# Optimization experiments

Hardware: AMD Instinct MI355X
Metric: run time of the kernel (lower is better)

Reference implementation:

```python
import jax, jax.numpy as jnp
import numpy as np

N = 100_000      # nodes
E = 1_600_000    # edges (before self-loops)
IN_C = 500
HID = 128
OUT_C = 64
L = 8
ALPHA = 0.1
THETA = 0.5


def setup_inputs() -> dict:
    key = jax.random.key(0)
    ks = jax.random.split(key, 6)
    x = jax.random.normal(ks[0], (N, IN_C), dtype=jnp.float32)
    edge_index = jax.random.randint(ks[1], (2, E), 0, N, dtype=jnp.int32)
    s0 = 1.0 / np.sqrt(IN_C)
    W_in = jax.random.uniform(ks[2], (IN_C, HID), jnp.float32, -s0, s0)
    b_in = jnp.zeros((HID,), jnp.float32)
    sh = 1.0 / np.sqrt(HID)
    W_conv = jax.random.uniform(ks[3], (L, HID, HID), jnp.float32, -sh, sh)
    W_out = jax.random.uniform(ks[4], (HID, OUT_C), jnp.float32, -sh, sh)
    b_out = jnp.zeros((OUT_C,), jnp.float32)
    return {"x": x, "edge_index": edge_index, "W_in": W_in, "b_in": b_in,
            "W_conv": W_conv, "W_out": W_out, "b_out": b_out}


def reference(x, edge_index, W_in, b_in, W_conv, W_out, b_out):
    # dropout is identity in eval mode
    loop = jnp.arange(N, dtype=edge_index.dtype)
    src = jnp.concatenate([edge_index[0], loop])  # add self-loops (gcn_norm)
    dst = jnp.concatenate([edge_index[1], loop])
    deg = jax.ops.segment_sum(jnp.ones_like(src, dtype=x.dtype), dst, num_segments=N)
    dinv = jnp.where(deg > 0, jax.lax.rsqrt(deg), 0.0)
    norm = dinv[src] * dinv[dst]  # symmetric normalization coeffs per edge

    h = jax.nn.relu(x @ W_in + b_in)
    h0 = h  # initial residual
    for l in range(L):
        beta = float(np.log(THETA / (l + 1) + 1.0))
        agg = jax.ops.segment_sum(h[src] * norm[:, None], dst, num_segments=N)  # Ahat @ h
        z = (1.0 - ALPHA) * agg + ALPHA * h0
        h = jax.nn.relu((1.0 - beta) * z + beta * (z @ W_conv[l]))
    return h @ W_out + b_out
```

## Files before the change

### kernel.cpp

```cpp
#include <hip/hip_runtime.h>
#include <hip/hip_fp16.h>
#include <cmath>

#define NN 100000
#define EE 1600000
#define INC 500
#define HIDC 128
#define OUTC 64
#define NLAYER 8
#define NB16 6250
#define NPX 12500
#define GEMM_BLKS 782
#define CNT_BLKS 50000
#define FG_BLKS (GEMM_BLKS + CNT_BLKS)

typedef float f32x4 __attribute__((ext_vector_type(4)));
typedef _Float16 f16x8 __attribute__((ext_vector_type(8)));
typedef _Float16 f16x4 __attribute__((ext_vector_type(4)));
typedef short s16x8 __attribute__((ext_vector_type(8)));

__device__ __forceinline__ int fraddr(int row, int k, int Kp) {
  return (row >> 4) * (Kp * 16) + (k >> 3) * 128 + (row & 15) * 8 + (k & 7);
}


__global__ void __launch_bounds__(256) k_count_x(
    const int* __restrict__ dst, int* __restrict__ deg) {
  int chunk = blockIdx.x >> 3;
  int xcd = blockIdx.x & 7;
  int e = chunk * 256 + threadIdx.x;
  int d = dst[e];
  if (d / NPX == xcd) atomicAdd(&deg[d], 1);
}

__global__ void k_scan_block_sums(const int* __restrict__ deg, int* __restrict__ bsum, int n) {
  __shared__ int sm[256];
  int i = blockIdx.x * 256 + threadIdx.x;
  int v = (i < n) ? deg[i] + 1 : 0;
  sm[threadIdx.x] = v;
  __syncthreads();
  for (int s = 128; s > 0; s >>= 1) {
    if (threadIdx.x < s) sm[threadIdx.x] += sm[threadIdx.x + s];
    __syncthreads();
  }
  if (threadIdx.x == 0) bsum[blockIdx.x] = sm[0];
}

__global__ void k_scan_partials(int* __restrict__ bsum, int nb) {
  __shared__ int sm[512];
  int t = threadIdx.x;
  sm[t] = (t < nb) ? bsum[t] : 0;
  __syncthreads();
  for (int s = 1; s < 512; s <<= 1) {
    int v = (t >= s) ? sm[t - s] : 0;
    __syncthreads();
    sm[t] += v;
    __syncthreads();
  }
  if (t < nb) bsum[t] = (t == 0) ? 0 : sm[t - 1];
}

__global__ void k_scan_final(const int* __restrict__ deg, const int* __restrict__ bsum,
                             int* __restrict__ row_ptr, int n) {
  __shared__ int sm[256];
  int i = blockIdx.x * 256 + threadIdx.x;
  int v = (i < n) ? deg[i] + 1 : 0;
  sm[threadIdx.x] = v;
  __syncthreads();
  for (int s = 1; s < 256; s <<= 1) {
    int u = (threadIdx.x >= s) ? sm[threadIdx.x - s] : 0;
    __syncthreads();
    sm[threadIdx.x] += u;
    __syncthreads();
  }
  if (i < n) row_ptr[i] = bsum[blockIdx.x] + sm[threadIdx.x] - v;
}

__global__ void k_init_rows(const int* __restrict__ deg, const int* __restrict__ row_ptr,
                            int* __restrict__ cursor, int* __restrict__ col,
                            float* __restrict__ dinv, int n) {
  int i = blockIdx.x * blockDim.x + threadIdx.x;
  if (i < n) {
    int rp = row_ptr[i];
    col[rp] = i;
    cursor[i] = rp + 1;
    dinv[i] = rsqrtf((float)(deg[i] + 1));
  }
}


__global__ void k_prep_wfin16(const float* __restrict__ W, __half* __restrict__ f) {
  int i = blockIdx.x * 256 + threadIdx.x;
  if (i >= HIDC * 512) return;
  int n = i / 512, k = i % 512;
  float v = (k < INC) ? W[(size_t)k * HIDC + n] : 0.f;
  f[fraddr(n, k, 512)] = __float2half(v);
}


__global__ void k_prep_wf16(const float* __restrict__ W, __half* __restrict__ f,
                            int K, int N, float idc, float ws) {
  int i = blockIdx.x * 256 + threadIdx.x;
  if (i >= N * K) return;
  int n = i / K, k = i % K;
  float v = ws * W[(size_t)k * N + n] + ((k == n) ? idc : 0.f);
  f[fraddr(n, k, K)] = __float2half(v);
}


__global__ void __launch_bounds__(256) k_fill_gemm(
    const int* __restrict__ src, const int* __restrict__ dst,
    int* __restrict__ cursor, int* __restrict__ col,
    const float* __restrict__ A, const __half* __restrict__ Bf,
    const float* __restrict__ bias,
    __half* __restrict__ C16u, __half* __restrict__ C16s,
    const float* __restrict__ dinv) {
  __shared__ __align__(16) _Float16 Ax[128 * 40];
  int bid = blockIdx.x;
  int tid = threadIdx.x;

  if (bid >= GEMM_BLKS) {
    int chunk = (bid - GEMM_BLKS) >> 3;
    int xcd = bid & 7;
    int e = chunk * 256 + tid;
    int d = dst[e];
    if (d / NPX == xcd) {
      int pos = atomicAdd(&cursor[d], 1);
      col[pos] = src[e];
    }
    return;
  }

  int wid = tid >> 6, lane = tid & 63;
  int wr = wid >> 1, wc = wid & 1;
  int lr = lane & 15, kg = lane >> 4;
  int row0 = bid * 128;

  f32x4 acc[4][4];
#pragma unroll
  for (int m = 0; m < 4; ++m)
#pragma unroll
    for (int n = 0; n < 4; ++n) acc[m][n] = {0.f, 0.f, 0.f, 0.f};

  float4 va[4];
  auto issue_loads = [&](int kt) {
#pragma unroll
    for (int p = 0; p < 4; ++p) {
      int idx = tid + p * 256;
      int r = idx >> 3, kq = idx & 7;
      int gr = row0 + r, gk = kt + kq * 4;
      va[p] = make_float4(0.f, 0.f, 0.f, 0.f);
      if (gr < NN && gk < INC) va[p] = *reinterpret_cast<const float4*>(&A[(size_t)gr * INC + gk]);
    }
  };

  issue_loads(0);
  for (int kt = 0; kt < 512; kt += 32) {
#pragma unroll
    for (int p = 0; p < 4; ++p) {
      int idx = tid + p * 256;
      int r = idx >> 3, kq = idx & 7;
      const float* vp = &va[p].x;
      f16x4 h4;
#pragma unroll
      for (int e = 0; e < 4; ++e) h4[e] = (_Float16)vp[e];
      *reinterpret_cast<f16x4*>(&Ax[r * 40 + kq * 4]) = h4;
    }
    __syncthreads();
    if (kt + 32 < 512) issue_loads(kt + 32);

    f16x8 af[4];
#pragma unroll
    for (int m = 0; m < 4; ++m) {
      int r = wr * 64 + m * 16 + lr;
      af[m] = *reinterpret_cast<const f16x8*>(&Ax[r * 40 + kg * 8]);
    }
#pragma unroll
    for (int n = 0; n < 4; ++n) {
      size_t bb = (size_t)(wc * 4 + n) * 8192 + (size_t)(kt / 8 + kg) * 128 + lr * 8;
      f16x8 b = *reinterpret_cast<const f16x8*>(&Bf[bb]);
#pragma unroll
      for (int m = 0; m < 4; ++m)
        acc[m][n] = __builtin_amdgcn_mfma_f32_16x16x32_f16(af[m], b, acc[m][n], 0, 0, 0);
    }
    __syncthreads();
  }

#pragma unroll
  for (int m = 0; m < 4; ++m) {
#pragma unroll
    for (int n = 0; n < 4; ++n) {
      int gc = wc * 64 + n * 16 + lr;
#pragma unroll
      for (int q = 0; q < 4; ++q) {
        int gr = row0 + wr * 64 + m * 16 + kg * 4 + q;
        if (gr < NN) {
          float v = fmaxf(acc[m][n][q] + bias[gc], 0.f);
          C16u[(size_t)gr * HIDC + gc] = __float2half(v);
          C16s[(size_t)gr * HIDC + gc] = __float2half(v * dinv[gr]);
        }
      }
    }
  }
}


template <int EPI>
__global__ void __launch_bounds__(1024) k_layer(
    const __half* __restrict__ hs, const __half* __restrict__ h0u,
    const __half* __restrict__ Bf,
    const int* __restrict__ row_ptr, const int* __restrict__ deg,
    const int* __restrict__ col, const float* __restrict__ dinv,
    __half* __restrict__ Cs,
    const __half* __restrict__ Bf2, const float* __restrict__ bias2,
    float* __restrict__ outp) {
  __shared__ __half zb[16 * 128];
  int wv = threadIdx.x >> 6, lane = threadIdx.x & 63;
  int g = lane >> 4;
  int fl = lane & 15;
  int row0 = blockIdx.x * 16;
  int node = row0 + wv;

  int start = row_ptr[node];
  int cnt = deg[node] + 1;

  float acc[8];
#pragma unroll
  for (int j = 0; j < 8; ++j) acc[j] = 0.f;

  for (int base = 0; base < cnt; base += 64) {
    int rem = cnt - base;
    if (rem > 64) rem = 64;
    int myc = col[start + base + (lane < rem ? lane : 0)];
    int nch = (rem + 3) >> 2;

    auto get = [&](int ch, s16x8& v, float& m) {
      int e = ch * 4 + g;
      int c = __shfl(myc, e & 63, 64);
      m = (e < rem) ? 1.f : 0.f;
      v = *reinterpret_cast<const s16x8*>(&hs[(size_t)c * HIDC + fl * 8]);
    };

    s16x8 curv; float curm;
    get(0, curv, curm);
    for (int ch = 0; ch < nch; ++ch) {
      s16x8 nv = {}; float nm = 0.f;
      if (ch + 1 < nch) get(ch + 1, nv, nm);
      const __half2* hp = reinterpret_cast<const __half2*>(&curv);
#pragma unroll
      for (int j = 0; j < 4; ++j) {
        float2 f = __half22float2(hp[j]);
        acc[2 * j]     = fmaf(curm, f.x, acc[2 * j]);
        acc[2 * j + 1] = fmaf(curm, f.y, acc[2 * j + 1]);
      }
      curv = nv; curm = nm;
    }
  }

#pragma unroll
  for (int j = 0; j < 8; ++j) {
    acc[j] += __shfl_xor(acc[j], 16, 64);
    acc[j] += __shfl_xor(acc[j], 32, 64);
  }

  if (g == 0) {
    float dr = dinv[node] * 0.9f;
    s16x8 r0 = *reinterpret_cast<const s16x8*>(&h0u[(size_t)node * HIDC + fl * 8]);
    const __half2* r0p = reinterpret_cast<const __half2*>(&r0);
    f16x8 w;
#pragma unroll
    for (int j = 0; j < 4; ++j) {
      float2 f0 = __half22float2(r0p[j]);
      w[2 * j]     = (_Float16)fmaf(dr, acc[2 * j],     0.1f * f0.x);
      w[2 * j + 1] = (_Float16)fmaf(dr, acc[2 * j + 1], 0.1f * f0.y);
    }
    *reinterpret_cast<f16x8*>(&zb[wv * 128 + ((fl * 8) ^ ((wv & 7) << 3))]) = w;
  }
  __syncthreads();

  int lr = lane & 15, kg = lane >> 4;
  f32x4 c = {0.f, 0.f, 0.f, 0.f};
  if (wv < 8) {
    const __half* Bb = Bf + wv * 2048 + kg * 128 + lr * 8;
#pragma unroll
    for (int kt = 0; kt < 4; ++kt) {
      f16x8 a = *reinterpret_cast<const f16x8*>(
          &zb[lr * 128 + ((kt * 32 + kg * 8) ^ ((lr & 7) << 3))]);
      f16x8 b = *reinterpret_cast<const f16x8*>(Bb + kt * 512);
      c = __builtin_amdgcn_mfma_f32_16x16x32_f16(a, b, c, 0, 0, 0);
    }
  }

  if (EPI == 0) {
    if (wv < 8) {
      int gc = wv * 16 + lr;
#pragma unroll
      for (int q = 0; q < 4; ++q) {
        int gr = row0 + kg * 4 + q;
        float v = fmaxf(c[q], 0.f);
        Cs[(size_t)gr * HIDC + gc] = __float2half(v * dinv[gr]);
      }
    }
  } else {
    __syncthreads();
    if (wv < 8) {
      int gc = wv * 16 + lr;
#pragma unroll
      for (int q = 0; q < 4; ++q) {
        int r = kg * 4 + q;
        zb[(gc >> 3) * 128 + r * 8 + (gc & 7)] = __float2half(fmaxf(c[q], 0.f));
      }
    }
    __syncthreads();
    if (wv < 4) {
      f32x4 o = {0.f, 0.f, 0.f, 0.f};
      const __half* Bb2 = Bf2 + wv * 2048 + kg * 128 + lr * 8;
#pragma unroll
      for (int kt = 0; kt < 4; ++kt) {
        f16x8 a = *reinterpret_cast<const f16x8*>(&zb[(kt * 4 + kg) * 128 + lr * 8]);
        f16x8 b = *reinterpret_cast<const f16x8*>(Bb2 + kt * 512);
        o = __builtin_amdgcn_mfma_f32_16x16x32_f16(a, b, o, 0, 0, 0);
      }
      int gc = wv * 16 + lr;
      float bv = bias2[gc];
#pragma unroll
      for (int q = 0; q < 4; ++q) {
        int gr = row0 + kg * 4 + q;
        outp[(size_t)gr * OUTC + gc] = o[q] + bv;
      }
    }
  }
}


extern "C" void kernel_launch(void* const* d_in, const int* in_sizes, int n_in,
                              void* d_out, int out_size, void* d_ws, size_t ws_size,
                              hipStream_t stream) {
  const float* x     = (const float*)d_in[0];
  const int*   ei    = (const int*)d_in[1];
  const float* W_in  = (const float*)d_in[2];
  const float* b_in  = (const float*)d_in[3];
  const float* W_cv  = (const float*)d_in[4];
  const float* W_out = (const float*)d_in[5];
  const float* b_out = (const float*)d_in[6];
  float* out = (float*)d_out;

  char* ws = (char*)d_ws;
  size_t off = 0;
  auto alloc = [&](size_t bytes) {
    char* p = ws + off;
    off = (off + bytes + 255) & ~(size_t)255;
    return p;
  };
  int*    deg     = (int*)alloc((size_t)NN * 4);
  int*    row_ptr = (int*)alloc((size_t)NN * 4);
  int*    cursor  = (int*)alloc((size_t)NN * 4);
  int*    bsum    = (int*)alloc(512 * 4);
  float*  dinv    = (float*)alloc((size_t)NN * 4);
  int*    col     = (int*)alloc((size_t)(EE + NN) * 4);
  __half* h016u   = (__half*)alloc((size_t)NN * HIDC * 2);
  __half* h016s   = (__half*)alloc((size_t)NN * HIDC * 2);
  __half* hsA     = (__half*)alloc((size_t)NN * HIDC * 2);
  __half* hsB     = (__half*)alloc((size_t)NN * HIDC * 2);
  __half* wcv16   = (__half*)alloc((size_t)NLAYER * HIDC * HIDC * 2);
  __half* wout16  = (__half*)alloc((size_t)OUTC * HIDC * 2);
  __half* win16   = (__half*)alloc((size_t)HIDC * 512 * 2);

  const int* srcp = ei;
  const int* dstp = ei + EE;

  hipMemsetAsync(deg, 0, (size_t)NN * 4, stream);

  k_prep_wfin16<<<(HIDC * 512 + 255) / 256, 256, 0, stream>>>(W_in, win16);
  for (int l = 0; l < NLAYER; ++l) {
    float beta = logf(0.5f / (float)(l + 1) + 1.0f);
    k_prep_wf16<<<(HIDC * HIDC + 255) / 256, 256, 0, stream>>>(
        W_cv + (size_t)l * HIDC * HIDC, wcv16 + (size_t)l * HIDC * HIDC,
        HIDC, HIDC, 1.0f - beta, beta);
  }
  k_prep_wf16<<<(OUTC * HIDC + 255) / 256, 256, 0, stream>>>(W_out, wout16, HIDC, OUTC,
                                                             0.f, 1.f);

  k_count_x<<<CNT_BLKS, 256, 0, stream>>>(dstp, deg);

  int nb = (NN + 255) / 256;
  k_scan_block_sums<<<nb, 256, 0, stream>>>(deg, bsum, NN);
  k_scan_partials<<<1, 512, 0, stream>>>(bsum, nb);
  k_scan_final<<<nb, 256, 0, stream>>>(deg, bsum, row_ptr, NN);
  k_init_rows<<<(NN + 255) / 256, 256, 0, stream>>>(deg, row_ptr, cursor, col, dinv, NN);

  k_fill_gemm<<<FG_BLKS, 256, 0, stream>>>(srcp, dstp, cursor, col,
                                           x, win16, b_in, h016u, h016s, dinv);

  const __half* hcur = h016s;
  for (int l = 0; l < NLAYER; ++l) {
    const __half* wl = wcv16 + (size_t)l * HIDC * HIDC;
    if (l < NLAYER - 1) {
      __half* tgt = (l & 1) ? hsB : hsA;
      k_layer<0><<<NB16, 1024, 0, stream>>>(hcur, h016u, wl, row_ptr, deg, col, dinv,
                                            tgt, nullptr, nullptr, nullptr);
      hcur = tgt;
    } else {
      k_layer<1><<<NB16, 1024, 0, stream>>>(hcur, h016u, wl, row_ptr, deg, col, dinv,
                                            nullptr, wout16, b_out, out);
    }
  }
}
```

Before: 923.5 us.

## Sort nodes by degree for balanced layer blocks and split fill/GEMM kernel

Builds a degree histogram and a counting-sort permutation so that each 16-node block in the layer kernel handles nodes of similar degree. This reduces wave imbalance inside 1024-thread blocks, where the slowest node sets the block's time. The fused fill+GEMM kernel is also split into two separate kernels. The trade-offs are extra small kernels, indirect perm lookups, and scattered output rows that break write coalescing. Node locality across blocks is also lost.

```diff
diff --git a/kernel.cpp b/kernel.cpp
--- a/kernel.cpp
+++ b/kernel.cpp
@@ -12,7 +12,6 @@
 #define NPX 12500
 #define GEMM_BLKS 782
 #define CNT_BLKS 50000
-#define FG_BLKS (GEMM_BLKS + CNT_BLKS)
 
 typedef float f32x4 __attribute__((ext_vector_type(4)));
 typedef _Float16 f16x8 __attribute__((ext_vector_type(8)));
@@ -89,6 +88,53 @@
 }
 
 
+__global__ void k_hist(const int* __restrict__ deg, int* __restrict__ hist) {
+  __shared__ int lh[64];
+  if (threadIdx.x < 64) lh[threadIdx.x] = 0;
+  __syncthreads();
+  int i = blockIdx.x * 256 + threadIdx.x;
+  if (i < NN) atomicAdd(&lh[min(deg[i], 63)], 1);
+  __syncthreads();
+  if (threadIdx.x < 64 && lh[threadIdx.x]) atomicAdd(&hist[threadIdx.x], lh[threadIdx.x]);
+}
+
+__global__ void k_scan_hist(const int* __restrict__ hist, int* __restrict__ bincur) {
+  __shared__ int sm[64];
+  int t = threadIdx.x;
+  sm[t] = hist[t];
+  __syncthreads();
+  for (int s = 1; s < 64; s <<= 1) {
+    int v = (t >= s) ? sm[t - s] : 0;
+    __syncthreads();
+    sm[t] += v;
+    __syncthreads();
+  }
+  bincur[t] = (t == 0) ? 0 : sm[t - 1];
+}
+
+__global__ void k_perm(const int* __restrict__ deg, int* __restrict__ bincur,
+                       int* __restrict__ perm) {
+  int i = blockIdx.x * 256 + threadIdx.x;
+  if (i < NN) {
+    int p = atomicAdd(&bincur[min(deg[i], 63)], 1);
+    perm[p] = i;
+  }
+}
+
+__global__ void __launch_bounds__(256) k_fill_x(
+    const int* __restrict__ src, const int* __restrict__ dst,
+    int* __restrict__ cursor, int* __restrict__ col) {
+  int chunk = blockIdx.x >> 3;
+  int xcd = blockIdx.x & 7;
+  int e = chunk * 256 + threadIdx.x;
+  int d = dst[e];
+  if (d / NPX == xcd) {
+    int pos = atomicAdd(&cursor[d], 1);
+    col[pos] = src[e];
+  }
+}
+
+
 __global__ void k_prep_wfin16(const float* __restrict__ W, __half* __restrict__ f) {
   int i = blockIdx.x * 256 + threadIdx.x;
   if (i >= HIDC * 512) return;
@@ -108,33 +154,17 @@
 }
 
 
-__global__ void __launch_bounds__(256) k_fill_gemm(
-    const int* __restrict__ src, const int* __restrict__ dst,
-    int* __restrict__ cursor, int* __restrict__ col,
+__global__ void __launch_bounds__(256) k_gemm_in(
     const float* __restrict__ A, const __half* __restrict__ Bf,
     const float* __restrict__ bias,
     __half* __restrict__ C16u, __half* __restrict__ C16s,
     const float* __restrict__ dinv) {
   __shared__ __align__(16) _Float16 Ax[128 * 40];
-  int bid = blockIdx.x;
   int tid = threadIdx.x;
-
-  if (bid >= GEMM_BLKS) {
-    int chunk = (bid - GEMM_BLKS) >> 3;
-    int xcd = bid & 7;
-    int e = chunk * 256 + tid;
-    int d = dst[e];
-    if (d / NPX == xcd) {
-      int pos = atomicAdd(&cursor[d], 1);
-      col[pos] = src[e];
-    }
-    return;
-  }
-
   int wid = tid >> 6, lane = tid & 63;
   int wr = wid >> 1, wc = wid & 1;
   int lr = lane & 15, kg = lane >> 4;
-  int row0 = bid * 128;
+  int row0 = blockIdx.x * 128;
 
   f32x4 acc[4][4];
 #pragma unroll
@@ -211,6 +241,7 @@
     const __half* __restrict__ Bf,
     const int* __restrict__ row_ptr, const int* __restrict__ deg,
     const int* __restrict__ col, const float* __restrict__ dinv,
+    const int* __restrict__ perm,
     __half* __restrict__ Cs,
     const __half* __restrict__ Bf2, const float* __restrict__ bias2,
     float* __restrict__ outp) {
@@ -219,7 +250,7 @@
   int g = lane >> 4;
   int fl = lane & 15;
   int row0 = blockIdx.x * 16;
-  int node = row0 + wv;
+  int node = perm[row0 + wv];
 
   int start = row_ptr[node];
   int cnt = deg[node] + 1;
@@ -296,9 +327,9 @@
       int gc = wv * 16 + lr;
 #pragma unroll
       for (int q = 0; q < 4; ++q) {
-        int gr = row0 + kg * 4 + q;
+        int pr = perm[row0 + kg * 4 + q];
         float v = fmaxf(c[q], 0.f);
-        Cs[(size_t)gr * HIDC + gc] = __float2half(v * dinv[gr]);
+        Cs[(size_t)pr * HIDC + gc] = __float2half(v * dinv[pr]);
       }
     }
   } else {
@@ -325,8 +356,8 @@
       float bv = bias2[gc];
 #pragma unroll
       for (int q = 0; q < 4; ++q) {
-        int gr = row0 + kg * 4 + q;
-        outp[(size_t)gr * OUTC + gc] = o[q] + bv;
+        int pr = perm[row0 + kg * 4 + q];
+        outp[(size_t)pr * OUTC + gc] = o[q] + bv;
       }
     }
   }
@@ -356,6 +387,9 @@
   int*    row_ptr = (int*)alloc((size_t)NN * 4);
   int*    cursor  = (int*)alloc((size_t)NN * 4);
   int*    bsum    = (int*)alloc(512 * 4);
+  int*    hist    = (int*)alloc(64 * 4);
+  int*    bincur  = (int*)alloc(64 * 4);
+  int*    perm    = (int*)alloc((size_t)NN * 4);
   float*  dinv    = (float*)alloc((size_t)NN * 4);
   int*    col     = (int*)alloc((size_t)(EE + NN) * 4);
   __half* h016u   = (__half*)alloc((size_t)NN * HIDC * 2);
@@ -370,6 +404,7 @@
   const int* dstp = ei + EE;
 
   hipMemsetAsync(deg, 0, (size_t)NN * 4, stream);
+  hipMemsetAsync(hist, 0, 64 * 4, stream);
 
   k_prep_wfin16<<<(HIDC * 512 + 255) / 256, 256, 0, stream>>>(W_in, win16);
   for (int l = 0; l < NLAYER; ++l) {
@@ -389,8 +424,13 @@
   k_scan_final<<<nb, 256, 0, stream>>>(deg, bsum, row_ptr, NN);
   k_init_rows<<<(NN + 255) / 256, 256, 0, stream>>>(deg, row_ptr, cursor, col, dinv, NN);
 
-  k_fill_gemm<<<FG_BLKS, 256, 0, stream>>>(srcp, dstp, cursor, col,
-                                           x, win16, b_in, h016u, h016s, dinv);
+  k_hist<<<nb, 256, 0, stream>>>(deg, hist);
+  k_scan_hist<<<1, 64, 0, stream>>>(hist, bincur);
+  k_perm<<<nb, 256, 0, stream>>>(deg, bincur, perm);
+
+  k_fill_x<<<CNT_BLKS, 256, 0, stream>>>(srcp, dstp, cursor, col);
+
+  k_gemm_in<<<GEMM_BLKS, 256, 0, stream>>>(x, win16, b_in, h016u, h016s, dinv);
 
   const __half* hcur = h016s;
   for (int l = 0; l < NLAYER; ++l) {
@@ -398,11 +438,11 @@
     if (l < NLAYER - 1) {
       __half* tgt = (l & 1) ? hsB : hsA;
       k_layer<0><<<NB16, 1024, 0, stream>>>(hcur, h016u, wl, row_ptr, deg, col, dinv,
-                                            tgt, nullptr, nullptr, nullptr);
+                                            perm, tgt, nullptr, nullptr, nullptr);
       hcur = tgt;
     } else {
       k_layer<1><<<NB16, 1024, 0, stream>>>(hcur, h016u, wl, row_ptr, deg, col, dinv,
-                                            nullptr, wout16, b_out, out);
-    }
-  }
-}
+                                            perm, nullptr, wout16, b_out, out);
+    }
+  }
+}
```

Result: slower. 1.193 ms (+29.2%).

## Split fused fill/GEMM kernel and use LDS-free per-wave input GEMM

Applied to the files above, without the earlier changes.

Separates the CSR column fill from the input projection GEMM, which were previously fused into one launch. The GEMM is rewritten so each wave computes 16 rows by all 128 columns, loading fp32 rows directly into registers without LDS staging or block barriers. The cost is an extra kernel launch and serialising the fill with the GEMM, which removes the overlap the fused launch allowed. Scan block count becomes a constant.

```diff
diff --git a/kernel.cpp b/kernel.cpp
--- a/kernel.cpp
+++ b/kernel.cpp
@@ -10,13 +10,11 @@
 #define NLAYER 8
 #define NB16 6250
 #define NPX 12500
-#define GEMM_BLKS 782
 #define CNT_BLKS 50000
-#define FG_BLKS (GEMM_BLKS + CNT_BLKS)
+#define NBLK 391
 
 typedef float f32x4 __attribute__((ext_vector_type(4)));
 typedef _Float16 f16x8 __attribute__((ext_vector_type(8)));
-typedef _Float16 f16x4 __attribute__((ext_vector_type(4)));
 typedef short s16x8 __attribute__((ext_vector_type(8)));
 
 __device__ __forceinline__ int fraddr(int row, int k, int Kp) {
@@ -88,6 +86,19 @@
   }
 }
 
+__global__ void __launch_bounds__(256) k_fill_x(
+    const int* __restrict__ src, const int* __restrict__ dst,
+    int* __restrict__ cursor, int* __restrict__ col) {
+  int chunk = blockIdx.x >> 3;
+  int xcd = blockIdx.x & 7;
+  int e = chunk * 256 + threadIdx.x;
+  int d = dst[e];
+  if (d / NPX == xcd) {
+    int pos = atomicAdd(&cursor[d], 1);
+    col[pos] = src[e];
+  }
+}
+
 
 __global__ void k_prep_wfin16(const float* __restrict__ W, __half* __restrict__ f) {
   int i = blockIdx.x * 256 + threadIdx.x;
@@ -108,98 +119,58 @@
 }
 
 
-__global__ void __launch_bounds__(256) k_fill_gemm(
-    const int* __restrict__ src, const int* __restrict__ dst,
-    int* __restrict__ cursor, int* __restrict__ col,
+__global__ void __launch_bounds__(256) k_gemm_in(
     const float* __restrict__ A, const __half* __restrict__ Bf,
     const float* __restrict__ bias,
     __half* __restrict__ C16u, __half* __restrict__ C16s,
     const float* __restrict__ dinv) {
-  __shared__ __align__(16) _Float16 Ax[128 * 40];
-  int bid = blockIdx.x;
-  int tid = threadIdx.x;
-
-  if (bid >= GEMM_BLKS) {
-    int chunk = (bid - GEMM_BLKS) >> 3;
-    int xcd = bid & 7;
-    int e = chunk * 256 + tid;
-    int d = dst[e];
-    if (d / NPX == xcd) {
-      int pos = atomicAdd(&cursor[d], 1);
-      col[pos] = src[e];
-    }
-    return;
-  }
-
-  int wid = tid >> 6, lane = tid & 63;
-  int wr = wid >> 1, wc = wid & 1;
+  int wv = threadIdx.x >> 6, lane = threadIdx.x & 63;
   int lr = lane & 15, kg = lane >> 4;
-  int row0 = bid * 128;
-
-  f32x4 acc[4][4];
-#pragma unroll
-  for (int m = 0; m < 4; ++m)
-#pragma unroll
-    for (int n = 0; n < 4; ++n) acc[m][n] = {0.f, 0.f, 0.f, 0.f};
-
-  float4 va[4];
-  auto issue_loads = [&](int kt) {
-#pragma unroll
-    for (int p = 0; p < 4; ++p) {
-      int idx = tid + p * 256;
-      int r = idx >> 3, kq = idx & 7;
-      int gr = row0 + r, gk = kt + kq * 4;
-      va[p] = make_float4(0.f, 0.f, 0.f, 0.f);
-      if (gr < NN && gk < INC) va[p] = *reinterpret_cast<const float4*>(&A[(size_t)gr * INC + gk]);
-    }
-  };
-
-  issue_loads(0);
-  for (int kt = 0; kt < 512; kt += 32) {
-#pragma unroll
-    for (int p = 0; p < 4; ++p) {
-      int idx = tid + p * 256;
-      int r = idx >> 3, kq = idx & 7;
-      const float* vp = &va[p].x;
-      f16x4 h4;
-#pragma unroll
-      for (int e = 0; e < 4; ++e) h4[e] = (_Float16)vp[e];
-      *reinterpret_cast<f16x4*>(&Ax[r * 40 + kq * 4]) = h4;
-    }
-    __syncthreads();
-    if (kt + 32 < 512) issue_loads(kt + 32);
-
-    f16x8 af[4];
-#pragma unroll
-    for (int m = 0; m < 4; ++m) {
-      int r = wr * 64 + m * 16 + lr;
-      af[m] = *reinterpret_cast<const f16x8*>(&Ax[r * 40 + kg * 8]);
-    }
-#pragma unroll
-    for (int n = 0; n < 4; ++n) {
-      size_t bb = (size_t)(wc * 4 + n) * 8192 + (size_t)(kt / 8 + kg) * 128 + lr * 8;
-      f16x8 b = *reinterpret_cast<const f16x8*>(&Bf[bb]);
-#pragma unroll
-      for (int m = 0; m < 4; ++m)
-        acc[m][n] = __builtin_amdgcn_mfma_f32_16x16x32_f16(af[m], b, acc[m][n], 0, 0, 0);
-    }
-    __syncthreads();
-  }
-
-#pragma unroll
-  for (int m = 0; m < 4; ++m) {
-#pragma unroll
-    for (int n = 0; n < 4; ++n) {
-      int gc = wc * 64 + n * 16 + lr;
-#pragma unroll
-      for (int q = 0; q < 4; ++q) {
-        int gr = row0 + wr * 64 + m * 16 + kg * 4 + q;
-        if (gr < NN) {
-          float v = fmaxf(acc[m][n][q] + bias[gc], 0.f);
-          C16u[(size_t)gr * HIDC + gc] = __float2half(v);
-          C16s[(size_t)gr * HIDC + gc] = __float2half(v * dinv[gr]);
-        }
-      }
+  int w16 = blockIdx.x * 4 + wv;
+  if (w16 >= NB16) return;
+  int row = w16 * 16 + lr;
+
+  f32x4 acc[8];
+#pragma unroll
+  for (int n = 0; n < 8; ++n) acc[n] = {0.f, 0.f, 0.f, 0.f};
+
+  const float* Ar = A + (size_t)row * INC;
+  const __half* Bb = Bf + lr * 8;
+
+#pragma unroll
+  for (int kt = 0; kt < 16; ++kt) {
+    int k0 = kt * 32 + kg * 8;
+    f16x8 af;
+    if (kt < 15 || kg < 2) {
+      float4 a0 = *reinterpret_cast<const float4*>(Ar + k0);
+      float4 a1 = *reinterpret_cast<const float4*>(Ar + k0 + 4);
+      af[0] = (_Float16)a0.x; af[1] = (_Float16)a0.y;
+      af[2] = (_Float16)a0.z; af[3] = (_Float16)a0.w;
+      af[4] = (_Float16)a1.x; af[5] = (_Float16)a1.y;
+      af[6] = (_Float16)a1.z; af[7] = (_Float16)a1.w;
+    } else {
+#pragma unroll
+      for (int e = 0; e < 8; ++e)
+        af[e] = (_Float16)((k0 + e < INC) ? Ar[k0 + e] : 0.f);
+    }
+    int kslab = (kt * 4 + kg) * 128;
+#pragma unroll
+    for (int n = 0; n < 8; ++n) {
+      f16x8 b = *reinterpret_cast<const f16x8*>(&Bb[n * 8192 + kslab]);
+      acc[n] = __builtin_amdgcn_mfma_f32_16x16x32_f16(af, b, acc[n], 0, 0, 0);
+    }
+  }
+
+#pragma unroll
+  for (int q = 0; q < 4; ++q) {
+    int gr = w16 * 16 + kg * 4 + q;
+    float dv = dinv[gr];
+#pragma unroll
+    for (int n = 0; n < 8; ++n) {
+      int gc = n * 16 + lr;
+      float v = fmaxf(acc[n][q] + bias[gc], 0.f);
+      C16u[(size_t)gr * HIDC + gc] = __float2half(v);
+      C16s[(size_t)gr * HIDC + gc] = __float2half(v * dv);
     }
   }
 }
@@ -383,14 +354,14 @@
 
   k_count_x<<<CNT_BLKS, 256, 0, stream>>>(dstp, deg);
 
-  int nb = (NN + 255) / 256;
-  k_scan_block_sums<<<nb, 256, 0, stream>>>(deg, bsum, NN);
-  k_scan_partials<<<1, 512, 0, stream>>>(bsum, nb);
-  k_scan_final<<<nb, 256, 0, stream>>>(deg, bsum, row_ptr, NN);
+  k_scan_block_sums<<<NBLK, 256, 0, stream>>>(deg, bsum, NN);
+  k_scan_partials<<<1, 512, 0, stream>>>(bsum, NBLK);
+  k_scan_final<<<NBLK, 256, 0, stream>>>(deg, bsum, row_ptr, NN);
   k_init_rows<<<(NN + 255) / 256, 256, 0, stream>>>(deg, row_ptr, cursor, col, dinv, NN);
 
-  k_fill_gemm<<<FG_BLKS, 256, 0, stream>>>(srcp, dstp, cursor, col,
-                                           x, win16, b_in, h016u, h016s, dinv);
+  k_fill_x<<<CNT_BLKS, 256, 0, stream>>>(srcp, dstp, cursor, col);
+
+  k_gemm_in<<<(NB16 + 3) / 4, 256, 0, stream>>>(x, win16, b_in, h016u, h016s, dinv);
 
   const __half* hcur = h016s;
   for (int l = 0; l < NLAYER; ++l) {
```

Result: no change. 912.1 us (-1.2%).
